# Optimization experiments

Measured on AMD Instinct MI355X. Metric: run time of the kernel, lower is better.

The kernel has to match this reference:

```python
import jax, jax.numpy as jnp
import numpy as np

B, T, C, H = 8, 2048, 1024, 16
N_LAYER, LAYER_ID = 12, 1
NH = C // H           # head size = 64
CHUNK = 256


def setup_inputs() -> dict:
    key = jax.random.key(0)
    ks = jax.random.split(key, 10)
    # deterministic init matching the torch __init__
    ratio_0_to_1 = LAYER_ID / (N_LAYER - 1)
    ratio_1_to_almost0 = 1.0 - LAYER_ID / N_LAYER
    ddd = np.arange(C, dtype=np.float32) / C
    time_maa_k = (1.0 - ddd ** ratio_1_to_almost0).astype(np.float32)
    time_maa_v = (1.0 - (ddd ** ratio_1_to_almost0 + 0.3 * ratio_0_to_1)).astype(np.float32)
    time_maa_r = (1.0 - ddd ** (0.5 * ratio_1_to_almost0)).astype(np.float32)
    h_idx = np.arange(H, dtype=np.float32)
    time_decay = (-6.0 + 5.0 * (h_idx / (H - 1)) ** (0.7 + 1.3 * ratio_0_to_1)).astype(np.float32)
    s = 0.02
    return {
        "x": jax.random.normal(ks[0], (B, T, C), jnp.float32),
        "volatility": jax.random.uniform(ks[1], (B, T), jnp.float32),
        "Wvol": jax.random.normal(ks[2], (C, 1), jnp.float32) * s,
        "bvol": jnp.zeros((C,), jnp.float32),
        "time_maa_k": jnp.asarray(time_maa_k),
        "time_maa_v": jnp.asarray(time_maa_v),
        "time_maa_r": jnp.asarray(time_maa_r),
        "time_decay": jnp.asarray(time_decay),
        "Wk": jax.random.normal(ks[3], (C, C), jnp.float32) * s,
        "Wv": jax.random.normal(ks[4], (C, C), jnp.float32) * s,
        "Wr": jax.random.normal(ks[5], (C, C), jnp.float32) * s,
        "Wo": jax.random.normal(ks[6], (C, C), jnp.float32) * s,
        "gn_w": 1.0 + jax.random.normal(ks[7], (C,), jnp.float32) * s,
        "gn_b": jax.random.normal(ks[8], (C,), jnp.float32) * s,
    }


def reference(x, volatility, Wvol, bvol, time_maa_k, time_maa_v, time_maa_r,
              time_decay, Wk, Wv, Wr, Wo, gn_w, gn_b):
    b, t, c = x.shape
    h = time_decay.shape[0]
    n = c // h
    nc = t // CHUNK

    # volatility gating: sigmoid(Linear(1->C))
    v_emb = jax.nn.sigmoid(volatility[:, :, None] * Wvol[:, 0] + bvol)  # (B,T,C)
    x = x * v_emb

    # time shift (zero-pad one step at the front, drop last)
    xx = jnp.pad(x, ((0, 0), (1, 0), (0, 0)))[:, :-1] - x
    xk = x + xx * time_maa_k
    xv = x + xx * time_maa_v
    xr = x + xx * time_maa_r

    r = (xr @ Wr.T).reshape(b, t, h, n).transpose(0, 2, 1, 3)  # (B,H,T,N)
    k = (xk @ Wk.T).reshape(b, t, h, n).transpose(0, 2, 1, 3)
    v = (xv @ Wv.T).reshape(b, t, h, n).transpose(0, 2, 1, 3)

    w = jnp.exp(-jnp.exp(time_decay))[None, :, None, None]  # scalar decay per head

    # chunked linear-attention recurrence (faithful to torch loop, chunk=256, no intra-chunk mask)
    rc = r.reshape(b, h, nc, CHUNK, n).transpose(2, 0, 1, 3, 4)  # (nc,B,H,CK,N)
    kc = k.reshape(b, h, nc, CHUNK, n).transpose(2, 0, 1, 3, 4)
    vc = v.reshape(b, h, nc, CHUNK, n).transpose(2, 0, 1, 3, 4)

    def step(state, rkv):
        rr, kk, vv = rkv  # each (B,H,CK,N)
        att = jnp.einsum('bhtn,bhsn->bhts', rr, kk)            # r @ k^T
        y = w * (jnp.einsum('bhts,bhsn->bhtn', att, vv)
                 + jnp.einsum('bhtn,bhnm->bhtm', rr, state))
        new_state = w * (state + jnp.einsum('bhsn,bhsm->bhnm', kk, vv))
        return new_state, y

    state0 = jnp.zeros((b, h, n, n), x.dtype)
    _, ys = jax.lax.scan(step, state0, (rc, kc, vc))            # (nc,B,H,CK,N)
    y = ys.transpose(1, 2, 0, 3, 4).reshape(b, h, t, n)
    y = y.transpose(0, 2, 1, 3).reshape(b * t, c)

    # GroupNorm with H groups over channels
    yg = y.reshape(b * t, h, n)
    mu = yg.mean(-1, keepdims=True)
    var = yg.var(-1, keepdims=True)
    yg = (yg - mu) * jax.lax.rsqrt(var + 1e-5)
    y = (yg.reshape(b * t, c) * gn_w + gn_b).reshape(b, t, c)

    return y @ Wo.T  # dropout is identity in eval
```

## Files before the change

kernel.cpp:

```cpp
#include <hip/hip_runtime.h>

typedef unsigned short u16;
typedef __attribute__((ext_vector_type(4))) unsigned int u32x4;
typedef __attribute__((ext_vector_type(4))) float f32x4;
typedef __attribute__((ext_vector_type(8))) short s16x8;

#define B_ 8
#define T_ 2048
#define C_ 1024
#define H_ 16
#define HS_ 64
#define CHUNK_ 256
#define NC_ 8

union U8 { u32x4 u; u16 h[8]; };

__device__ __forceinline__ float b2f(u16 v) {
    union { unsigned int i; float f; } c; c.i = ((unsigned int)v) << 16; return c.f;
}
__device__ __forceinline__ u16 f2b(float f) {
    union { float f; unsigned int i; } c; c.f = f;
    unsigned int i = c.i;
    return (u16)((i + 0x7FFFu + ((i >> 16) & 1u)) >> 16);
}
__device__ __forceinline__ float fsig(float z) {
    return __builtin_amdgcn_rcpf(1.f + __expf(-z));
}

typedef __attribute__((address_space(1))) void GV;
typedef __attribute__((address_space(3))) void LV;
__device__ __forceinline__ void glds16(const void* g, void* l) {
    __builtin_amdgcn_global_load_lds((GV*)g, (LV*)l, 16, 0, 0);
}

__global__ __launch_bounds__(256) void cvt4_kernel(
    const float* __restrict__ s0, const float* __restrict__ s1,
    const float* __restrict__ s2, const float* __restrict__ s3,
    u16* __restrict__ dst)
{
    int i = blockIdx.x * 256 + threadIdx.x;
    int m = i >> 17;
    const float* s = (m == 0) ? s0 : (m == 1) ? s1 : (m == 2) ? s2 : s3;
    size_t j = (size_t)(i & 131071) * 8;
    f32x4 a = *reinterpret_cast<const f32x4*>(s + j);
    f32x4 b = *reinterpret_cast<const f32x4*>(s + j + 4);
    U8 o;
    #pragma unroll
    for (int k = 0; k < 4; k++) { o.h[k] = f2b(a[k]); o.h[4 + k] = f2b(b[k]); }
    *reinterpret_cast<u32x4*>(dst + (size_t)m * C_ * C_ + j) = o.u;
}

__global__ __launch_bounds__(256) void mix_kernel(
    const float* __restrict__ x, const float* __restrict__ vol,
    const float* __restrict__ Wvol, const float* __restrict__ bvol,
    const float* __restrict__ mk, const float* __restrict__ mv, const float* __restrict__ mr,
    u16* __restrict__ xk, u16* __restrict__ xv, u16* __restrict__ xr)
{
    int idx = blockIdx.x * 256 + threadIdx.x;
    int c0 = (idx & 127) * 8;
    int bt8 = idx >> 7;
    int t0  = (bt8 & 255) * 8;
    int b   = bt8 >> 8;
    size_t rowOff = ((size_t)b * T_ + t0) * C_ + c0;

    float wv[8], bv[8], mkv[8], mvv[8], mrv[8];
    #pragma unroll
    for (int j = 0; j < 8; j += 4) {
        f32x4 a;
        a = *reinterpret_cast<const f32x4*>(Wvol + c0 + j);
        wv[j] = a[0]; wv[j+1] = a[1]; wv[j+2] = a[2]; wv[j+3] = a[3];
        a = *reinterpret_cast<const f32x4*>(bvol + c0 + j);
        bv[j] = a[0]; bv[j+1] = a[1]; bv[j+2] = a[2]; bv[j+3] = a[3];
        a = *reinterpret_cast<const f32x4*>(mk + c0 + j);
        mkv[j] = a[0]; mkv[j+1] = a[1]; mkv[j+2] = a[2]; mkv[j+3] = a[3];
        a = *reinterpret_cast<const f32x4*>(mv + c0 + j);
        mvv[j] = a[0]; mvv[j+1] = a[1]; mvv[j+2] = a[2]; mvv[j+3] = a[3];
        a = *reinterpret_cast<const f32x4*>(mr + c0 + j);
        mrv[j] = a[0]; mrv[j+1] = a[1]; mrv[j+2] = a[2]; mrv[j+3] = a[3];
    }

    const float* volb = vol + (size_t)b * T_;
    float gp[8];
    if (t0 == 0) {
        #pragma unroll
        for (int j = 0; j < 8; j++) gp[j] = 0.f;
    } else {
        float vp = volb[t0 - 1];
        #pragma unroll
        for (int j = 0; j < 8; j += 4) {
            f32x4 a = *reinterpret_cast<const f32x4*>(x + rowOff - C_ + j);
            gp[j]   = a[0] * fsig(vp * wv[j]   + bv[j]);
            gp[j+1] = a[1] * fsig(vp * wv[j+1] + bv[j+1]);
            gp[j+2] = a[2] * fsig(vp * wv[j+2] + bv[j+2]);
            gp[j+3] = a[3] * fsig(vp * wv[j+3] + bv[j+3]);
        }
    }

    #pragma unroll
    for (int s = 0; s < 8; s++) {
        float vc = volb[t0 + s];
        size_t off = rowOff + (size_t)s * C_;
        float g[8];
        #pragma unroll
        for (int j = 0; j < 8; j += 4) {
            f32x4 a = *reinterpret_cast<const f32x4*>(x + off + j);
            g[j]   = a[0] * fsig(vc * wv[j]   + bv[j]);
            g[j+1] = a[1] * fsig(vc * wv[j+1] + bv[j+1]);
            g[j+2] = a[2] * fsig(vc * wv[j+2] + bv[j+2]);
            g[j+3] = a[3] * fsig(vc * wv[j+3] + bv[j+3]);
        }
        U8 ok, ov, orr;
        #pragma unroll
        for (int j = 0; j < 8; j++) {
            float xx = gp[j] - g[j];
            ok.h[j]  = f2b(g[j] + xx * mkv[j]);
            ov.h[j]  = f2b(g[j] + xx * mvv[j]);
            orr.h[j] = f2b(g[j] + xx * mrv[j]);
            gp[j] = g[j];
        }
        *reinterpret_cast<u32x4*>(xk + off) = ok.u;
        *reinterpret_cast<u32x4*>(xv + off) = ov.u;
        *reinterpret_cast<u32x4*>(xr + off) = orr.u;
    }
}

#define GBM_ 256
#define GBN_ 256
#define GBK_ 32
#define GK_  1024
#define GNT_ 32
#define GEMM_LDS_BYTES 131072

template<bool F32OUT>
__global__ __launch_bounds__(512, 2) void gemm_bt(
    const u16* __restrict__ A, const u16* __restrict__ W, void* __restrict__ Cc)
{
    extern __shared__ __align__(16) u16 lds[];
    const int tid  = threadIdx.x;
    const int lane = tid & 63, w = tid >> 6;
    const int r16  = lane & 15, quad = lane >> 4;
    const int wm2  = w >> 2;
    const int wn4  = w & 3;
    const int id   = blockIdx.x;
    const int bm   = id & 63, bn = id >> 6;

    const u16* Ab = A + (size_t)bm * GBM_ * GK_;
    const u16* Wb = W + (size_t)bn * GBN_ * GK_;

    const int srow   = lane >> 2;
    const int schunk = ((lane & 3) ^ ((lane >> 3) & 3)) * 8;
    const u16* aS0 = Ab + (size_t)(w * 32 + srow) * GK_ + schunk;
    const u16* aS1 = aS0 + (size_t)16 * GK_;
    const u16* bS0 = Wb + (size_t)(w * 32 + srow) * GK_ + schunk;
    const u16* bS1 = bS0 + (size_t)16 * GK_;
    u16* aD0 = lds + (w * 32) * 32;
    u16* aD1 = aD0 + 16 * 32;
    u16* bD0 = lds + 32768 + (w * 32) * 32;
    u16* bD1 = bD0 + 16 * 32;

    const int ksw = (quad ^ ((r16 >> 1) & 3)) * 8;
    int aOff[8], bOff[4];
    #pragma unroll
    for (int mi = 0; mi < 8; mi++)
        aOff[mi] = (wm2 * 128 + mi * 16 + r16) * 32 + ksw;
    #pragma unroll
    for (int ni = 0; ni < 4; ni++)
        bOff[ni] = 32768 + (wn4 * 64 + ni * 16 + r16) * 32 + ksw;

    f32x4 acc[8][4];
    #pragma unroll
    for (int mi = 0; mi < 8; mi++)
        #pragma unroll
        for (int ni = 0; ni < 4; ni++)
            acc[mi][ni] = f32x4{0.f, 0.f, 0.f, 0.f};

#define STG(tt) {                                                        \
    const int bo_ = ((tt) & 3) * 8192;                                   \
    const size_t ko_ = (size_t)(tt) * 32;                                \
    glds16(aS0 + ko_, aD0 + bo_);                                        \
    glds16(aS1 + ko_, aD1 + bo_);                                        \
    glds16(bS0 + ko_, bD0 + bo_);                                        \
    glds16(bS1 + ko_, bD1 + bo_);                                        \
}

    STG(0);
    STG(1);
    asm volatile("s_waitcnt vmcnt(4)" ::: "memory");
    __builtin_amdgcn_s_barrier();
    asm volatile("" ::: "memory");

    for (int s = 0; s < GNT_; ++s) {
        const int bo = (s & 3) * 8192;
        if (s + 2 < GNT_) STG(s + 2);

        s16x8 fb[4];
        #pragma unroll
        for (int ni = 0; ni < 4; ni++)
            fb[ni] = *reinterpret_cast<const s16x8*>(lds + bo + bOff[ni]);
        __builtin_amdgcn_s_setprio(1);
        #pragma unroll
        for (int mi = 0; mi < 8; mi++) {
            s16x8 fa = *reinterpret_cast<const s16x8*>(lds + bo + aOff[mi]);
            #pragma unroll
            for (int ni = 0; ni < 4; ni++)
                acc[mi][ni] = __builtin_amdgcn_mfma_f32_16x16x32_bf16(
                    fa, fb[ni], acc[mi][ni], 0, 0, 0);
        }
        __builtin_amdgcn_s_setprio(0);

        if (s + 2 < GNT_) asm volatile("s_waitcnt vmcnt(4)" ::: "memory");
        else              asm volatile("s_waitcnt vmcnt(0)" ::: "memory");
        __builtin_amdgcn_s_barrier();
        asm volatile("" ::: "memory");
    }
#undef STG

    if constexpr (F32OUT) {
        float* C = (float*)Cc;
        #pragma unroll
        for (int mi = 0; mi < 8; mi++) {
            int row0 = bm * GBM_ + wm2 * 128 + mi * 16 + quad * 4;
            #pragma unroll
            for (int ni = 0; ni < 4; ni++) {
                int col = bn * GBN_ + wn4 * 64 + ni * 16 + r16;
                #pragma unroll
                for (int i = 0; i < 4; i++)
                    C[(size_t)(row0 + i) * C_ + col] = acc[mi][ni][i];
            }
        }
    } else {
        u16* ep = lds + w * 4608;
        u16* C = (u16*)Cc;
        #pragma unroll
        for (int half = 0; half < 2; half++) {
            #pragma unroll
            for (int mi2 = 0; mi2 < 4; mi2++) {
                int mi = half * 4 + mi2;
                #pragma unroll
                for (int ni = 0; ni < 4; ni++)
                    #pragma unroll
                    for (int i = 0; i < 4; i++)
                        ep[(mi2 * 16 + quad * 4 + i) * 72 + ni * 16 + r16] =
                            f2b(acc[mi][ni][i]);
            }
            #pragma unroll
            for (int it = 0; it < 8; it++) {
                int rr = it * 8 + (lane >> 3);
                u32x4 val = *reinterpret_cast<const u32x4*>(ep + rr * 72 + (lane & 7) * 8);
                size_t grow = (size_t)(bm * GBM_ + wm2 * 128 + half * 64 + rr);
                *reinterpret_cast<u32x4*>(
                    C + grow * C_ + bn * GBN_ + wn4 * 64 + (lane & 7) * 8) = val;
            }
        }
    }
}

__global__ __launch_bounds__(256) void kvouter_kernel(
    const u16* __restrict__ k, const u16* __restrict__ v, float* __restrict__ S)
{
    int blk = blockIdx.x;
    int j  = blk & (NC_ - 1);
    int bh = blk >> 3;
    int h = bh & (H_ - 1);
    int b = bh >> 4;
    __shared__ __align__(16) u16 kT[HS_ * 136];
    __shared__ __align__(16) u16 vT[HS_ * 136];
    int tid = threadIdx.x, lane = tid & 63, wave = tid >> 6;
    int r16 = lane & 15, quad = lane >> 4;
    int n0 = (wave >> 1) * 32, m0 = (wave & 1) * 32;
    int a = tid & 7, c8 = a * 8;

    f32x4 acc[2][2];
    #pragma unroll
    for (int ni = 0; ni < 2; ni++)
        #pragma unroll
        for (int mi = 0; mi < 2; mi++)
            acc[ni][mi] = f32x4{0.f, 0.f, 0.f, 0.f};

    size_t base = ((size_t)(b * T_ + j * CHUNK_)) * C_ + h * HS_;
    #pragma unroll
    for (int half = 0; half < 2; half++) {
        size_t hb = base + (size_t)half * 128 * C_;
        #pragma unroll
        for (int i = 0; i < 4; i++) {
            int s = (tid + i * 256) >> 3;
            U8 uk, uv;
            uk.u = *reinterpret_cast<const u32x4*>(k + hb + (size_t)s * C_ + c8);
            uv.u = *reinterpret_cast<const u32x4*>(v + hb + (size_t)s * C_ + c8);
            #pragma unroll
            for (int jj = 0; jj < 8; jj++) {
                int w = jj ^ a;
                kT[(c8 + w) * 136 + s] = uk.h[w];
                vT[(c8 + w) * 136 + s] = uv.h[w];
            }
        }
        __syncthreads();
        #pragma unroll
        for (int ks = 0; ks < 4; ks++) {
            s16x8 fa[2], fb[2];
            #pragma unroll
            for (int ni = 0; ni < 2; ni++)
                fa[ni] = *reinterpret_cast<const s16x8*>(
                    &vT[(n0 + ni * 16 + r16) * 136 + ks * 32 + quad * 8]);
            #pragma unroll
            for (int mi = 0; mi < 2; mi++)
                fb[mi] = *reinterpret_cast<const s16x8*>(
                    &kT[(m0 + mi * 16 + r16) * 136 + ks * 32 + quad * 8]);
            #pragma unroll
            for (int ni = 0; ni < 2; ni++)
                #pragma unroll
                for (int mi = 0; mi < 2; mi++)
                    acc[ni][mi] = __builtin_amdgcn_mfma_f32_16x16x32_bf16(fa[ni], fb[mi], acc[ni][mi], 0, 0, 0);
        }
        __syncthreads();
    }
    float* out = S + (size_t)blk * (HS_ * HS_);
    #pragma unroll
    for (int ni = 0; ni < 2; ni++)
        #pragma unroll
        for (int mi = 0; mi < 2; mi++)
            #pragma unroll
            for (int i = 0; i < 4; i++)
                out[(n0 + ni * 16 + quad * 4 + i) * HS_ + m0 + mi * 16 + r16] = acc[ni][mi][i];
}

__global__ __launch_bounds__(256) void scan_kernel(
    const float* __restrict__ S, const float* __restrict__ td, u16* __restrict__ stT)
{
    int bh = blockIdx.x;
    int h = bh & (H_ - 1);
    float w = expf(-expf(td[h]));
    int tid = threadIdx.x;
    float st[16];
    #pragma unroll
    for (int i = 0; i < 16; i++) st[i] = 0.f;
    for (int c = 0; c < NC_; c++) {
        size_t off = ((size_t)(bh * NC_ + c)) * 4096 + tid * 16;
        const float* sp = S + off;
        #pragma unroll
        for (int i = 0; i < 16; i++) st[i] = w * (st[i] + sp[i]);
        U8 o0, o1;
        #pragma unroll
        for (int i = 0; i < 8; i++) { o0.h[i] = f2b(st[i]); o1.h[i] = f2b(st[8 + i]); }
        *reinterpret_cast<u32x4*>(stT + off)     = o0.u;
        *reinterpret_cast<u32x4*>(stT + off + 8) = o1.u;
    }
}

__global__ __launch_bounds__(256) void rstate_gn_kernel(
    const u16* __restrict__ r, const u16* __restrict__ stT,
    const float* __restrict__ gnw, const float* __restrict__ gnb, u16* __restrict__ ygn)
{
    int blk = blockIdx.x;
    int c  = blk & (NC_ - 1);
    int bh = blk >> 3;
    int h = bh & (H_ - 1);
    int b = bh >> 4;
    __shared__ __align__(16) u16 sT[HS_ * 72];
    int tid = threadIdx.x, lane = tid & 63, wave = tid >> 6;
    int r16 = lane & 15, quad = lane >> 4;

    const u16* sg = stT + (size_t)blk * (HS_ * HS_);
    for (int i = tid; i < 512; i += 256) {
        int n = i >> 3, c8 = (i & 7) * 8;
        *reinterpret_cast<u32x4*>(&sT[n * 72 + c8]) =
            *reinterpret_cast<const u32x4*>(sg + n * HS_ + c8);
    }
    __syncthreads();

    size_t rowBase = (size_t)(b * T_ + c * CHUNK_ + wave * 64);
    f32x4 acc[4][4];
    #pragma unroll
    for (int mi = 0; mi < 4; mi++)
        #pragma unroll
        for (int ni = 0; ni < 4; ni++)
            acc[mi][ni] = f32x4{0.f, 0.f, 0.f, 0.f};

    #pragma unroll
    for (int ks = 0; ks < 2; ks++) {
        int kb = ks * 32 + quad * 8;
        s16x8 fa[4], fb[4];
        #pragma unroll
        for (int mi = 0; mi < 4; mi++)
            fa[mi] = *reinterpret_cast<const s16x8*>(
                r + (rowBase + mi * 16 + r16) * C_ + h * HS_ + kb);
        #pragma unroll
        for (int ni = 0; ni < 4; ni++)
            fb[ni] = *reinterpret_cast<const s16x8*>(&sT[(ni * 16 + r16) * 72 + kb]);
        #pragma unroll
        for (int mi = 0; mi < 4; mi++)
            #pragma unroll
            for (int ni = 0; ni < 4; ni++)
                acc[mi][ni] = __builtin_amdgcn_mfma_f32_16x16x32_bf16(fa[mi], fb[ni], acc[mi][ni], 0, 0, 0);
    }

    float gwv[4], gbv[4];
    #pragma unroll
    for (int ni = 0; ni < 4; ni++) {
        int col = ni * 16 + r16;
        gwv[ni] = gnw[h * HS_ + col];
        gbv[ni] = gnb[h * HS_ + col];
    }
    #pragma unroll
    for (int mi = 0; mi < 4; mi++) {
        float s1[4], s2[4];
        #pragma unroll
        for (int i = 0; i < 4; i++) {
            float s = 0.f, ss = 0.f;
            #pragma unroll
            for (int ni = 0; ni < 4; ni++) {
                float v = acc[mi][ni][i];
                s += v; ss += v * v;
            }
            s1[i] = s; s2[i] = ss;
        }
        #pragma unroll
        for (int d = 1; d < 16; d <<= 1) {
            #pragma unroll
            for (int i = 0; i < 4; i++) {
                s1[i] += __shfl_xor(s1[i], d);
                s2[i] += __shfl_xor(s2[i], d);
            }
        }
        #pragma unroll
        for (int i = 0; i < 4; i++) {
            float mu = s1[i] * (1.f / 64.f);
            float var = s2[i] * (1.f / 64.f) - mu * mu;
            float sc = rsqrtf(var + 1e-5f);
            size_t ob = (rowBase + mi * 16 + quad * 4 + i) * C_ + h * HS_;
            #pragma unroll
            for (int ni = 0; ni < 4; ni++)
                ygn[ob + ni * 16 + r16] = f2b((acc[mi][ni][i] - mu) * sc * gwv[ni] + gbv[ni]);
        }
    }
}

extern "C" void kernel_launch(void* const* d_in, const int* in_sizes, int n_in,
                              void* d_out, int out_size, void* d_ws, size_t ws_size,
                              hipStream_t stream) {
    const float* x    = (const float*)d_in[0];
    const float* vol  = (const float*)d_in[1];
    const float* Wvol = (const float*)d_in[2];
    const float* bvol = (const float*)d_in[3];
    const float* mk   = (const float*)d_in[4];
    const float* mv   = (const float*)d_in[5];
    const float* mr   = (const float*)d_in[6];
    const float* td   = (const float*)d_in[7];
    const float* Wk   = (const float*)d_in[8];
    const float* Wv   = (const float*)d_in[9];
    const float* Wr   = (const float*)d_in[10];
    const float* Wo   = (const float*)d_in[11];
    const float* gnw  = (const float*)d_in[12];
    const float* gnb  = (const float*)d_in[13];
    float* out = (float*)d_out;

    static bool init_attr = []() {
        hipFuncSetAttribute(reinterpret_cast<const void*>(gemm_bt<false>),
                            hipFuncAttributeMaxDynamicSharedMemorySize, GEMM_LDS_BYTES);
        hipFuncSetAttribute(reinterpret_cast<const void*>(gemm_bt<true>),
                            hipFuncAttributeMaxDynamicSharedMemorySize, GEMM_LDS_BYTES);
        return true;
    }();
    (void)init_attr;

    char* ws = (char*)d_ws;
    const size_t SLOT = (size_t)B_ * T_ * C_ * 2;
    u16* xr = (u16*)(ws + 0 * SLOT);
    u16* xk = (u16*)(ws + 1 * SLOT);
    u16* xv = (u16*)(ws + 2 * SLOT);
    u16* rb = (u16*)(ws + 3 * SLOT);
    u16* kb = (u16*)(ws + 0 * SLOT);
    u16* vb = (u16*)(ws + 1 * SLOT);
    float* S   = (float*)(ws + 2 * SLOT);
    u16*   stT = (u16*)  (ws + 2 * SLOT + SLOT / 2);
    u16* ygn = (u16*)(ws + 0 * SLOT);
    u16* wtb = (u16*)(ws + 4 * SLOT);
    u16* wrb = wtb;
    u16* wkb = wrb + (size_t)C_ * C_;
    u16* wvb = wkb + (size_t)C_ * C_;
    u16* wob = wvb + (size_t)C_ * C_;

    cvt4_kernel<<<dim3(4 * (C_ * C_ / 8) / 256), dim3(256), 0, stream>>>(Wr, Wk, Wv, Wo, wtb);

    mix_kernel<<<dim3(1024), dim3(256), 0, stream>>>(
        x, vol, Wvol, bvol, mk, mv, mr, xk, xv, xr);

    gemm_bt<false><<<dim3(256), dim3(512), GEMM_LDS_BYTES, stream>>>(xr, wrb, rb);
    gemm_bt<false><<<dim3(256), dim3(512), GEMM_LDS_BYTES, stream>>>(xk, wkb, kb);
    gemm_bt<false><<<dim3(256), dim3(512), GEMM_LDS_BYTES, stream>>>(xv, wvb, vb);

    kvouter_kernel<<<dim3(B_ * H_ * NC_), dim3(256), 0, stream>>>(kb, vb, S);
    scan_kernel<<<dim3(B_ * H_), dim3(256), 0, stream>>>(S, td, stT);
    rstate_gn_kernel<<<dim3(B_ * H_ * NC_), dim3(256), 0, stream>>>(rb, stT, gnw, gnb, ygn);

    gemm_bt<true><<<dim3(256), dim3(512), GEMM_LDS_BYTES, stream>>>(ygn, wob, out);
}
```

Measured before the change: 383.1 us.

## Restructure GEMM main loop into BK=64 double-buffered phased schedule

Doubles the K tile from 32 to 64 and replaces the 4-stage ring of 32-wide tiles with two 64-wide buffers. Each iteration is split into four barrier-separated phases that interleave LDS fragment loads, global-to-LDS prefetch of the next tile and MFMA groups, with a new XOR swizzle for 64-element rows. The aim is fewer loop iterations and a more explicit overlap of memory and compute. The cost is many more barriers per iteration, and prefetch depth drops to one tile ahead.

```diff
diff --git a/kernel.cpp b/kernel.cpp
--- a/kernel.cpp
+++ b/kernel.cpp
@@ -126,9 +126,9 @@
 
 #define GBM_ 256
 #define GBN_ 256
-#define GBK_ 32
+#define GBK_ 64
 #define GK_  1024
-#define GNT_ 32
+#define GNT_ 16
 #define GEMM_LDS_BYTES 131072
 
 template<bool F32OUT>
@@ -147,25 +147,15 @@
     const u16* Ab = A + (size_t)bm * GBM_ * GK_;
     const u16* Wb = W + (size_t)bn * GBN_ * GK_;
 
-    const int srow   = lane >> 2;
-    const int schunk = ((lane & 3) ^ ((lane >> 3) & 3)) * 8;
-    const u16* aS0 = Ab + (size_t)(w * 32 + srow) * GK_ + schunk;
-    const u16* aS1 = aS0 + (size_t)16 * GK_;
-    const u16* bS0 = Wb + (size_t)(w * 32 + srow) * GK_ + schunk;
-    const u16* bS1 = bS0 + (size_t)16 * GK_;
-    u16* aD0 = lds + (w * 32) * 32;
-    u16* aD1 = aD0 + 16 * 32;
-    u16* bD0 = lds + 32768 + (w * 32) * 32;
-    u16* bD1 = bD0 + 16 * 32;
-
-    const int ksw = (quad ^ ((r16 >> 1) & 3)) * 8;
-    int aOff[8], bOff[4];
-    #pragma unroll
-    for (int mi = 0; mi < 8; mi++)
-        aOff[mi] = (wm2 * 128 + mi * 16 + r16) * 32 + ksw;
-    #pragma unroll
-    for (int ni = 0; ni < 4; ni++)
-        bOff[ni] = 32768 + (wn4 * 64 + ni * 16 + r16) * 32 + ksw;
+    const int srow8  = lane >> 3;
+    const int schunk = ((lane & 7) ^ srow8) * 8;
+    const u16* aSrc = Ab + (size_t)(w * 16 + srow8) * GK_ + schunk;
+    const u16* bSrc = Wb + (size_t)(w * 16 + srow8) * GK_ + schunk;
+
+    const int fA0 = (wm2 * 128 + r16) * 64;
+    const int fB0 = 16384 + (wn4 * 64 + r16) * 64;
+    const int c0 = ((quad)     ^ (r16 & 7)) * 8;
+    const int c1 = ((quad | 4) ^ (r16 & 7)) * 8;
 
     f32x4 acc[8][4];
     #pragma unroll
@@ -174,46 +164,58 @@
         for (int ni = 0; ni < 4; ni++)
             acc[mi][ni] = f32x4{0.f, 0.f, 0.f, 0.f};
 
-#define STG(tt) {                                                        \
-    const int bo_ = ((tt) & 3) * 8192;                                   \
-    const size_t ko_ = (size_t)(tt) * 32;                                \
-    glds16(aS0 + ko_, aD0 + bo_);                                        \
-    glds16(aS1 + ko_, aD1 + bo_);                                        \
-    glds16(bS0 + ko_, bD0 + bo_);                                        \
-    glds16(bS1 + ko_, bD1 + bo_);                                        \
-}
-
-    STG(0);
-    STG(1);
-    asm volatile("s_waitcnt vmcnt(4)" ::: "memory");
-    __builtin_amdgcn_s_barrier();
-    asm volatile("" ::: "memory");
-
-    for (int s = 0; s < GNT_; ++s) {
-        const int bo = (s & 3) * 8192;
-        if (s + 2 < GNT_) STG(s + 2);
-
-        s16x8 fb[4];
-        #pragma unroll
-        for (int ni = 0; ni < 4; ni++)
-            fb[ni] = *reinterpret_cast<const s16x8*>(lds + bo + bOff[ni]);
-        __builtin_amdgcn_s_setprio(1);
-        #pragma unroll
-        for (int mi = 0; mi < 8; mi++) {
-            s16x8 fa = *reinterpret_cast<const s16x8*>(lds + bo + aOff[mi]);
-            #pragma unroll
-            for (int ni = 0; ni < 4; ni++)
-                acc[mi][ni] = __builtin_amdgcn_mfma_f32_16x16x32_bf16(
-                    fa, fb[ni], acc[mi][ni], 0, 0, 0);
-        }
-        __builtin_amdgcn_s_setprio(0);
-
-        if (s + 2 < GNT_) asm volatile("s_waitcnt vmcnt(4)" ::: "memory");
-        else              asm volatile("s_waitcnt vmcnt(0)" ::: "memory");
-        __builtin_amdgcn_s_barrier();
-        asm volatile("" ::: "memory");
-    }
-#undef STG
+#define STQ(tt, h) do {                                                       \
+    const size_t ko_ = (size_t)(tt) * 64;                                     \
+    u16* db_ = lds + (((tt) & 1) * 32768) + ((h) * 128 + w * 16) * 64;        \
+    glds16(aSrc + (size_t)((h) * 128)     * GK_ + ko_, db_);                  \
+    glds16(aSrc + (size_t)((h) * 128 + 8) * GK_ + ko_, db_ + 512);            \
+    glds16(bSrc + (size_t)((h) * 128)     * GK_ + ko_, db_ + 16384);          \
+    glds16(bSrc + (size_t)((h) * 128 + 8) * GK_ + ko_, db_ + 16384 + 512);    \
+} while (0)
+
+#define PH_BAR() do { asm volatile("" ::: "memory");                          \
+    __builtin_amdgcn_s_barrier(); asm volatile("" ::: "memory"); } while (0)
+#define PH_LGKM0() do { asm volatile("s_waitcnt lgkmcnt(0)" ::: "memory");    \
+    __builtin_amdgcn_sched_barrier(0); } while (0)
+#define LDFA(CO) { _Pragma("unroll") for (int mi = 0; mi < 8; mi++)           \
+    fa[mi] = *reinterpret_cast<const s16x8*>(lds + pb + fA0 + mi * 1024 + (CO)); }
+#define LDFB(NH, CO) { _Pragma("unroll") for (int ni = 0; ni < 2; ni++)       \
+    fb[ni] = *reinterpret_cast<const s16x8*>(lds + pb + fB0 + ((NH) * 2 + ni) * 1024 + (CO)); }
+#define MFMA16(NH) do { __builtin_amdgcn_s_setprio(1);                        \
+    _Pragma("unroll") for (int mi = 0; mi < 8; mi++) {                        \
+        acc[mi][(NH)*2+0] = __builtin_amdgcn_mfma_f32_16x16x32_bf16(          \
+            fa[mi], fb[0], acc[mi][(NH)*2+0], 0, 0, 0);                       \
+        acc[mi][(NH)*2+1] = __builtin_amdgcn_mfma_f32_16x16x32_bf16(          \
+            fa[mi], fb[1], acc[mi][(NH)*2+1], 0, 0, 0);                       \
+    } __builtin_amdgcn_s_setprio(0); } while (0)
+
+    STQ(0, 0);
+    STQ(0, 1);
+    asm volatile("s_waitcnt vmcnt(0)" ::: "memory");
+    PH_BAR();
+
+    for (int t = 0; t < GNT_; ++t) {
+        const int pb = (t & 1) * 32768;
+        s16x8 fa[8], fb[2];
+        LDFA(c0); LDFB(0, c0);
+        if (t + 1 < GNT_) STQ(t + 1, 0);
+        PH_BAR(); PH_LGKM0(); MFMA16(0); PH_BAR();
+        LDFB(1, c0);
+        PH_BAR(); PH_LGKM0(); MFMA16(1); PH_BAR();
+        LDFA(c1); LDFB(0, c1);
+        if (t + 1 < GNT_) STQ(t + 1, 1);
+        PH_BAR(); PH_LGKM0(); MFMA16(0); PH_BAR();
+        LDFB(1, c1);
+        PH_BAR(); PH_LGKM0(); MFMA16(1);
+        asm volatile("s_waitcnt vmcnt(0)" ::: "memory");
+        PH_BAR();
+    }
+#undef STQ
+#undef LDFA
+#undef LDFB
+#undef MFMA16
+#undef PH_LGKM0
+#undef PH_BAR
 
     if constexpr (F32OUT) {
         float* C = (float*)Cc;
```

Result: faster. 373.8 us (-2.4%).
